# Kernel tuning notes

Measured on AMD Instinct MI355X. Metric: run time of the kernel, lower is better.

## Reference

```python
import jax, jax.numpy as jnp
import numpy as np

E = 256
CH = 16  # channel rows; features viewed as (16,16)


def _sigmoid_np(x):
    return 1.0 / (1.0 + np.exp(-x))


def _schedule(emb, comp_l, comp_r, cb, seqs):
    """Phase 1 (host/numpy, mirrors the detached torch control flow):
    runs the iterative argmax-merge tree construction and records the
    integer merge schedule (new composed node pairs per iteration) and the
    (target, ctx_left, ctx_right) prediction triples. Matches Banyan.compose."""
    emb = np.asarray(emb, np.float32)
    sl = _sigmoid_np(np.asarray(comp_l, np.float32))
    sr = _sigmoid_np(np.asarray(comp_r, np.float32))
    cbn = np.asarray(cb, np.float32)
    seqs = np.asarray(seqs, np.int64)

    uniq = np.unique(seqs)
    lookup = np.zeros(uniq.max() + 1, np.int64)
    lookup[uniq] = np.arange(len(uniq))
    lookup[uniq[-1]] = -1  # max unique value acts as pad sentinel (lookup[-1] = -1)
    index = lookup[seqs].copy()
    tokens = uniq[:-1]

    nodes = emb[tokens]  # detached node features used only for similarity / schedule

    def comp(f):  # f: (K,2,16,16)
        return (f[:, 0] * sl + f[:, 1] * sr + cbn).reshape(f.shape[0], -1)

    pair_src = np.zeros((0, 2), np.int64)
    pair_dst = np.zeros((0,), np.int64)
    new_pairs, targets = [], []
    B, W = index.shape

    while W != 1:
        valid = index != -1
        f = nodes[np.clip(index, 0, None)]              # (B,W,E)
        a, b = f[:, :-1], f[:, 1:]
        na = np.linalg.norm(a, axis=-1)
        nb = np.linalg.norm(b, axis=-1)
        cos = (a * b).sum(-1) / np.maximum(na * nb, 1e-8)
        cos = np.where(valid[:, 1:], cos, -np.inf)       # right slot padded -> -inf
        ms_all = np.argmax(cos, axis=1)
        active = ~np.all(index[:, 1:] == -1, axis=1)
        rows = np.nonzero(active)[0]
        ms = ms_all[rows]
        lp, rp = ms, ms + 1
        src = np.stack([index[rows, lp], index[rows, rp]], 1)  # (A,2)

        # dedup against existing composed pairs, then unique new pairs (sorted)
        if pair_src.shape[0] > 0 and src.shape[0] > 0:
            exists = (src[:, None, :] == pair_src[None]).all(-1).any(1)
            newp = src[~exists]
        else:
            newp = src
        if newp.shape[0] > 0:
            newp = np.unique(newp, axis=0)
        base = nodes.shape[0]
        if newp.shape[0] > 0:
            nodes = np.concatenate([nodes, comp(nodes[newp].reshape(-1, 2, CH, CH))], 0)
            pair_src = np.concatenate([pair_src, newp], 0)
            pair_dst = np.concatenate([pair_dst, base + np.arange(newp.shape[0])], 0)
        new_pairs.append(newp.astype(np.int64))

        # neighbourhood targets (get_neighbours): l_t block then r_t block
        lefts, rights = src[:, 0], src[:, 1]
        ls = index[rows, lp - 1].copy()
        ls[lp - 1 == -1] = -1
        rs = index[rows, np.minimum(rp + 1, W - 1)].copy()
        rs[rp + 1 == W] = -2
        targets.append(np.stack([lefts, ls, rights], 1))
        targets.append(np.stack([rights, lefts, rs], 1))

        # point both merged slots at the (possibly shared) composed node id
        if src.shape[0] > 0:
            eq = (src[:, None, :] == pair_src[None]).all(-1)
            nid = pair_dst[eq.argmax(1)]
            index[rows, lp] = nid
            index[rows, rp] = nid

        # reduce frontier: active rows drop the left merge slot, inactive drop last col
        keep = np.ones_like(index, dtype=bool)
        keep[rows, ms] = False
        keep[~active, -1] = False
        index = index[keep].reshape(B, W - 1)
        W -= 1

    targets = np.concatenate(targets, 0).astype(np.int64)
    return tokens, new_pairs, targets


def _replay(emb, comp_l, comp_r, cb, sos, eos, tokens, new_pairs, targets):
    """Phase 2 (jax, differentiable): rebuild node features following the
    recorded schedule, then compute the context->target cross entropy."""
    sl = jax.nn.sigmoid(comp_l)
    sr = jax.nn.sigmoid(comp_r)
    feats = emb[tokens]                                    # (n_tok, E)
    for p in new_pairs:
        if p.shape[0] == 0:
            continue
        f = feats[p].reshape(-1, 2, CH, CH)                # (K,2,16,16)
        feats = jnp.concatenate([feats, (f[:, 0] * sl + f[:, 1] * sr + cb).reshape(-1, E)], 0)
    feats = jnp.concatenate([feats, eos[None, :], sos[None, :]], 0)
    N = feats.shape[0]
    t = np.where(targets < 0, targets + N, targets)        # wrap -1 -> sos, -2 -> eos
    l = feats[t[:, 1]].reshape(-1, CH, CH)
    r = feats[t[:, 2]].reshape(-1, CH, CH)
    outs = (l * sl + r * sr + cb).reshape(-1, E)           # (T,E)
    logits = outs @ feats.T                                # (T,N)
    logp = jax.nn.log_softmax(logits, axis=-1)
    return -jnp.mean(logp[jnp.arange(t.shape[0]), t[:, 0]])


def setup_inputs() -> dict:
    key = jax.random.key(0)
    k1, k2, k3, k4, k5, k6, k7 = jax.random.split(key, 7)
    V, B, L = 30000, 64, 64
    tok = jax.random.randint(k1, (B, L), 0, V - 1, dtype=jnp.int32)
    lengths = jax.random.randint(k2, (B,), L // 2, L + 1, dtype=jnp.int32)
    lengths = lengths.at[0].set(L // 2)  # guarantee pad token (V-1) is present
    x = jnp.where(jnp.arange(L)[None, :] < lengths[:, None], tok, V - 1)
    return {
        "x": x,
        "emb": jax.random.normal(k3, (V, E), jnp.float32),
        "comp_l": jax.random.uniform(k4, (CH,), jnp.float32, 0.6, 0.9),
        "comp_r": jax.random.uniform(k5, (CH,), jnp.float32, 0.6, 0.9),
        "cb": jnp.zeros((CH,), jnp.float32),
        "sos": 0.02 * jax.random.normal(k6, (E,), jnp.float32),
        "eos": 0.02 * jax.random.normal(k7, (E,), jnp.float32),
    }


def reference(x, emb, comp_l, comp_r, cb, sos, eos):
    tokens, new_pairs, targets = _schedule(emb, comp_l, comp_r, cb, x)
    return _replay(emb, comp_l, comp_r, cb, sos, eos, tokens, new_pairs, targets)
```

## Files before the change

### kernel.cpp

```cpp
#include <hip/hip_runtime.h>
#include <math.h>


#define NMAX 8192
#define PRES 30720
#define HBITS 13
#define HSIZE 8192
#define HMASK 8191
#define LOG2E 1.44269504f
#define LN2 0.69314718f

typedef float f32x4 __attribute__((ext_vector_type(4)));
typedef short short8 __attribute__((ext_vector_type(8)));

__device__ __forceinline__ unsigned hash0(int key) {
    return (((unsigned)key) * 2654435761u) >> (32 - HBITS);
}

__device__ __forceinline__ unsigned short f2bf(float f) {
    unsigned u = __float_as_uint(f);
    unsigned r = ((u >> 16) & 1u) + 0x7FFFu;
    return (unsigned short)((u + r) >> 16);
}

__device__ __forceinline__ float rdl_f(float v, int lane) {
    return __int_as_float(__builtin_amdgcn_readlane(__float_as_int(v), lane));
}

#define SUM_STEP(CTRL, X) \
    X += __int_as_float(__builtin_amdgcn_update_dpp(0, __float_as_int(X), CTRL, 0xF, 0xF, true));
#define SUM3_REDUCE(A, B, C) {                                                  \
    SUM_STEP(0x121, A) SUM_STEP(0x121, B) SUM_STEP(0x121, C)                    \
    SUM_STEP(0x122, A) SUM_STEP(0x122, B) SUM_STEP(0x122, C)                    \
    SUM_STEP(0x124, A) SUM_STEP(0x124, B) SUM_STEP(0x124, C)                    \
    SUM_STEP(0x128, A) SUM_STEP(0x128, B) SUM_STEP(0x128, C)                    \
    A = rdl_f(A, 0) + rdl_f(A, 16) + rdl_f(A, 32) + rdl_f(A, 48);               \
    B = rdl_f(B, 0) + rdl_f(B, 16) + rdl_f(B, 32) + rdl_f(B, 48);               \
    C = rdl_f(C, 0) + rdl_f(C, 16) + rdl_f(C, 32) + rdl_f(C, 48);               \
}
#define ARGMAX_STEP(CTRL, V, I) {                                               \
    float _ov = __int_as_float(__builtin_amdgcn_update_dpp(0, __float_as_int(V), CTRL, 0xF, 0xF, true)); \
    int _oi = __builtin_amdgcn_update_dpp(0, I, CTRL, 0xF, 0xF, true);          \
    if (_ov > V || (_ov == V && _oi < I)) { V = _ov; I = _oi; }                 \
}
#define ARGMAX_REDUCE(V, I) {                                                   \
    ARGMAX_STEP(0x121, V, I) ARGMAX_STEP(0x122, V, I)                           \
    ARGMAX_STEP(0x124, V, I) ARGMAX_STEP(0x128, V, I)                           \
    float _v0 = rdl_f(V, 0), _v1 = rdl_f(V, 16), _v2 = rdl_f(V, 32), _v3 = rdl_f(V, 48); \
    int _i0 = __builtin_amdgcn_readlane(I, 0), _i1 = __builtin_amdgcn_readlane(I, 16);   \
    int _i2 = __builtin_amdgcn_readlane(I, 32), _i3 = __builtin_amdgcn_readlane(I, 48);  \
    V = _v0; I = _i0;                                                           \
    if (_v1 > V || (_v1 == V && _i1 < I)) { V = _v1; I = _i1; }                 \
    if (_v2 > V || (_v2 == V && _i2 < I)) { V = _v2; I = _i2; }                 \
    if (_v3 > V || (_v3 == V && _i3 < I)) { V = _v3; I = _i3; }                 \
}

__global__ __launch_bounds__(1024) void prep_kernel(
    const int* __restrict__ x, int* __restrict__ tokens,
    int* __restrict__ meta, int* __restrict__ index_g) {
    __shared__ int pres[PRES];
    __shared__ int part[1024];
    int tid = threadIdx.x;
    for (int i = tid; i < PRES; i += 1024) pres[i] = 0;
    __syncthreads();
    for (int i = tid; i < 4096; i += 1024) pres[x[i]] = 1;
    __syncthreads();
    int base = tid * 30;
    int loc[30];
    int s = 0;
#pragma unroll
    for (int i = 0; i < 30; ++i) { loc[i] = s; s += pres[base + i]; }
    part[tid] = s;
    __syncthreads();
    for (int off = 1; off < 1024; off <<= 1) {
        int v = (tid >= off) ? part[tid - off] : 0;
        __syncthreads();
        part[tid] += v;
        __syncthreads();
    }
    int excl = (tid == 0) ? 0 : part[tid - 1];
    int total = part[1023];
#pragma unroll
    for (int i = 0; i < 30; ++i) {
        if (pres[base + i]) tokens[excl + loc[i]] = base + i;
    }
    if (tid == 0) { meta[0] = total; meta[1] = total - 1; }
    for (int i = tid; i < 4096; i += 1024) {
        int t = x[i];
        int th = t / 30;
        int b2 = th * 30, off = t - b2;
        int r = (th ? part[th - 1] : 0);
        for (int j = 0; j < off; ++j) r += pres[b2 + j];
        index_g[i] = (r == total - 1) ? -1 : r;
    }
}

__global__ void copy_feats_kernel(const float* __restrict__ emb, const int* __restrict__ tokens,
                                  const int* __restrict__ meta, float* __restrict__ feats,
                                  float* __restrict__ norms) {
    int n = blockIdx.x;
    if (n >= meta[1]) return;
    int t = tokens[n];
    int k = threadIdx.x;
    const float4* src = (const float4*)(emb + (size_t)t * 256);
    float4* dst = (float4*)(feats + (size_t)n * 256);
    float4 v = src[k];
    dst[k] = v;
    float ss = v.x * v.x + v.y * v.y + v.z * v.z + v.w * v.w;
#pragma unroll
    for (int off = 32; off >= 1; off >>= 1) ss += __shfl_down(ss, off);
    if (k == 0) norms[n] = sqrtf(ss);
}

__global__ void init_cos_kernel(const float* __restrict__ feats, const float* __restrict__ norms,
                                const int* __restrict__ index_g, float* __restrict__ cos_g) {
    int bid = blockIdx.x;
    int b = bid / 63, j = bid % 63;
    int l = index_g[b * 64 + j], r = index_g[b * 64 + j + 1];
    float c = -INFINITY;
    if (r != -1) {
        int k = threadIdx.x;
        const float4* fa = (const float4*)(feats + (size_t)l * 256);
        const float4* fb = (const float4*)(feats + (size_t)r * 256);
        float4 a = fa[k], bb = fb[k];
        float d = a.x * bb.x + a.y * bb.y + a.z * bb.z + a.w * bb.w;
#pragma unroll
        for (int off = 32; off >= 1; off >>= 1) d += __shfl_down(d, off);
        c = d / fmaxf(norms[l] * norms[r], 1e-8f);
    }
    if (threadIdx.x == 0) cos_g[b * 64 + j] = c;
}


__global__ __launch_bounds__(64) void treebuild_kernel(
    const float* __restrict__ feats, const float* __restrict__ norms_g,
    const int* __restrict__ index_g, const float* __restrict__ cos_g,
    float* __restrict__ rowfeats, int4* __restrict__ rec,
    const float* __restrict__ comp_l, const float* __restrict__ comp_r,
    const float* __restrict__ cb) {
    __shared__ float lf[127][256];
    __shared__ int4 s_rec[63];
    int b = blockIdx.x;
    int lane = threadIdx.x;
    int c0 = 4 * (lane & 3);
    float4 sl4 = make_float4(1.f / (1.f + __expf(-comp_l[c0])),
                             1.f / (1.f + __expf(-comp_l[c0 + 1])),
                             1.f / (1.f + __expf(-comp_l[c0 + 2])),
                             1.f / (1.f + __expf(-comp_l[c0 + 3])));
    float4 sr4 = make_float4(1.f / (1.f + __expf(-comp_r[c0])),
                             1.f / (1.f + __expf(-comp_r[c0 + 1])),
                             1.f / (1.f + __expf(-comp_r[c0 + 2])),
                             1.f / (1.f + __expf(-comp_r[c0 + 3])));
    float4 cb4 = make_float4(cb[c0], cb[c0 + 1], cb[c0 + 2], cb[c0 + 3]);

    int gid = index_g[b * 64 + lane];
    int isreal = (gid >= 0) ? 1 : 0;
    for (int j = 0; j < 64; ++j) {
        int g = index_g[b * 64 + j];
        int gc = g < 0 ? 0 : g;
        ((float4*)&lf[j][0])[lane] = ((const float4*)(feats + (size_t)gc * 256))[lane];
    }
    float n0 = (gid >= 0) ? norms_g[gid] : 0.f;
    float n1 = 0.f;
    float cosr = (lane < 63) ? cos_g[b * 64 + lane] : -INFINITY;
    int locid = lane;
    unsigned long long alive = ~0ull;
    int nreal = 64 - __popcll(__ballot(gid < 0));

    float Mv = cosr; int Mi = lane;
    ARGMAX_REDUCE(Mv, Mi);

    for (int it = 0; it < 63; ++it) {
        int act = (nreal >= 2) ? 1 : 0;
        int p = Mi;
        unsigned long long after = (alive >> 1) >> p;
        int q = (p + 1 + __builtin_ctzll(after | 0x8000000000000000ull)) & 63;
        unsigned long long bel = alive & ((1ull << p) - 1ull);
        int pp = bel ? (63 - __builtin_clzll(bel)) : -1;
        unsigned long long aft2 = (q < 63) ? (alive >> (q + 1)) : 0ull;
        int ssp = aft2 ? (q + 1 + __builtin_ctzll(aft2)) : -1;
        int l_loc = __builtin_amdgcn_readlane(locid, p);
        int r_loc = __builtin_amdgcn_readlane(locid, q);
        int lsl = __builtin_amdgcn_readlane(locid, pp < 0 ? 0 : pp);
        int rsl = __builtin_amdgcn_readlane(locid, ssp < 0 ? 0 : ssp);
        int ls_loc = (pp >= 0) ? lsl : -1;
        int rs_loc = (ssp >= 0) ? rsl : -2;
        int Creal = (ssp >= 0) ? __builtin_amdgcn_readlane(isreal, ssp) : 0;
        if (lane == 0)
            s_rec[it] = make_int4(act ? l_loc : -9, r_loc, ls_loc, rs_loc);
        if (act) {
            float4 a = ((const float4*)&lf[l_loc][0])[lane];
            float4 bb = ((const float4*)&lf[r_loc][0])[lane];
            float4 av = (pp >= 0) ? ((const float4*)&lf[ls_loc < 0 ? 0 : ls_loc][0])[lane]
                                  : make_float4(0.f, 0.f, 0.f, 0.f);
            float4 cv = Creal ? ((const float4*)&lf[rs_loc < 0 ? 0 : rs_loc][0])[lane]
                              : make_float4(0.f, 0.f, 0.f, 0.f);
            float mv = (lane == p || lane == q || lane == pp) ? -INFINITY : cosr;
            float Mv2 = mv; int Mi2 = lane;
            ARGMAX_REDUCE(Mv2, Mi2);
            int nl = 64 + it;
            float4 v;
            v.x = a.x * sl4.x + bb.x * sr4.x + cb4.x;
            v.y = a.y * sl4.y + bb.y * sr4.y + cb4.y;
            v.z = a.z * sl4.z + bb.z * sr4.z + cb4.z;
            v.w = a.w * sl4.w + bb.w * sr4.w + cb4.w;
            ((float4*)&lf[nl][0])[lane] = v;
            float sv = v.x * v.x + v.y * v.y + v.z * v.z + v.w * v.w;
            float da = av.x * v.x + av.y * v.y + av.z * v.z + av.w * v.w;
            float dc = cv.x * v.x + cv.y * v.y + cv.z * v.z + cv.w * v.w;
            SUM3_REDUCE(sv, da, dc);
            float nn = sqrtf(sv);
            if (lane == it) n1 = nn;
            float nA = 1.f, nC = 1.f;
            if (pp >= 0) nA = (ls_loc < 64) ? rdl_f(n0, ls_loc) : rdl_f(n1, ls_loc - 64);
            if (Creal)   nC = (rs_loc < 64) ? rdl_f(n0, rs_loc) : rdl_f(n1, rs_loc - 64);
            float cosA = da / fmaxf(nA * nn, 1e-8f);
            float cosC = Creal ? (dc / fmaxf(nn * nC, 1e-8f)) : -INFINITY;
            if (lane == p) { cosr = cosC; locid = nl; }
            if (lane == pp) cosr = cosA;
            if (lane == q) cosr = -INFINITY;
            if (pp >= 0 && (cosA > Mv2 || (cosA == Mv2 && pp < Mi2))) { Mv2 = cosA; Mi2 = pp; }
            if (cosC > Mv2 || (cosC == Mv2 && p < Mi2)) { Mv2 = cosC; Mi2 = p; }
            Mv = Mv2; Mi = Mi2;
            alive &= ~(1ull << q);
            nreal -= 1;
        }
    }
    for (int it = 0; it < 63; ++it) {
        ((float4*)(rowfeats + ((size_t)b * 63 + it) * 256))[lane] =
            ((const float4*)&lf[64 + it][0])[lane];
    }
    if (lane < 63) rec[b * 63 + lane] = s_rec[lane];
}


__global__ __launch_bounds__(64) void idassign_kernel(
    const int4* __restrict__ rec, const int* __restrict__ index_g,
    int* __restrict__ targets, int* __restrict__ meta, int* __restrict__ newsrc) {
    __shared__ int s_map[64][128];
    __shared__ int s_hk[HSIZE], s_hv[HSIZE];
    int b = threadIdx.x;
    for (int i = b; i < HSIZE; i += 64) s_hk[i] = -1;
    for (int i = b; i < 4096; i += 64) s_map[i >> 6][i & 63] = index_g[i];
    int N0 = meta[1];
    int Ncur = N0, Tcur = 0;
    __syncthreads();
    int4 R = rec[b * 63];
    for (int it = 0; it < 63; ++it) {
        int4 Rn = R;
        if (it + 1 < 63) Rn = rec[b * 63 + it + 1];
        int act = (R.x != -9) ? 1 : 0;
        int l_g = 0, r_g = 0, key = 0, nid = 0;
        int ls_g = -1, rs_g = -2;
        unsigned h = 0;
        int won = 0, need = 0;
        if (act) {
            l_g = s_map[b][R.x];
            r_g = s_map[b][R.y];
            ls_g = (R.z >= 0) ? s_map[b][R.z] : R.z;
            rs_g = (R.w >= 0) ? s_map[b][R.w] : R.w;
            key = (l_g << HBITS) | r_g;
            h = hash0(key);
            need = 1;
        }
        while (__any(need)) {
            if (need) {
                int prev = atomicCAS(&s_hk[h], -1, key);
                if (prev == -1) { won = 1; need = 0; }
                else if (prev == key) { need = 0; }
                else { h = (h + 1) & HMASK; }
            }
        }
        unsigned long long actmask = __ballot(act != 0);
        unsigned long long winmask = __ballot(won != 0);
        unsigned long long below = (1ull << b) - 1ull;
        int ar = __popcll(actmask & below);
        int nact = __popcll(actmask);
        int newc = __popcll(winmask);
        if (won) {
            nid = Ncur + __popcll(winmask & below);
            s_hv[h] = nid;
        }
        __syncthreads();
        if (act && !won) nid = s_hv[h];
        if (won) newsrc[nid - N0] = (b << 6) | it;
        if (act) {
            int o1 = Tcur + ar;
            targets[o1 * 3 + 0] = l_g;
            targets[o1 * 3 + 1] = ls_g;
            targets[o1 * 3 + 2] = r_g;
            int o2 = Tcur + nact + ar;
            targets[o2 * 3 + 0] = r_g;
            targets[o2 * 3 + 1] = l_g;
            targets[o2 * 3 + 2] = rs_g;
            s_map[b][64 + it] = nid;
        }
        Ncur += newc;
        Tcur += 2 * nact;
        R = Rn;
    }
    if (b == 0) { meta[2] = Ncur; meta[3] = Tcur; meta[4] = Ncur - N0; }
}


__global__ __launch_bounds__(64) void materialize_kernel(
    const float* __restrict__ rowfeats, const int* __restrict__ newsrc,
    const int* __restrict__ meta, float* __restrict__ feats,
    const float* __restrict__ eos, const float* __restrict__ sos) {
    int g = blockIdx.x;
    int lane = threadIdx.x;
    if (g == 4032) {
        int n = meta[2];
        ((float4*)(feats + (size_t)n * 256))[lane] = ((const float4*)eos)[lane];
        ((float4*)(feats + (size_t)(n + 1) * 256))[lane] = ((const float4*)sos)[lane];
        return;
    }
    if (g >= meta[4]) return;
    int pk = newsrc[g];
    int b = pk >> 6, it = pk & 63;
    int N0 = meta[1];
    ((float4*)(feats + (size_t)(N0 + g) * 256))[lane] =
        ((const float4*)(rowfeats + ((size_t)b * 63 + it) * 256))[lane];
}

__global__ __launch_bounds__(256) void convert_feats_kernel(
    const float* __restrict__ feats, short8* __restrict__ fhT) {
    int g = blockIdx.x * 256 + threadIdx.x;
    int tile = g >> 9, rem = g & 511;
    int ks = rem >> 6, lane64 = rem & 63;
    int kq = lane64 >> 4, col = lane64 & 15;
    int row = tile * 16 + col;
    int e0 = (ks * 4 + kq) * 8;
    const float4* src = (const float4*)(feats + (size_t)row * 256 + e0);
    float4 v0 = src[0], v1 = src[1];
    short8 o;
    o[0] = (short)f2bf(v0.x); o[1] = (short)f2bf(v0.y);
    o[2] = (short)f2bf(v0.z); o[3] = (short)f2bf(v0.w);
    o[4] = (short)f2bf(v1.x); o[5] = (short)f2bf(v1.y);
    o[6] = (short)f2bf(v1.z); o[7] = (short)f2bf(v1.w);
    fhT[g] = o;
}

__global__ __launch_bounds__(256) void prep_outs_kernel(
    const float* __restrict__ feats, const int* __restrict__ targets,
    const int* __restrict__ meta, const float* __restrict__ comp_l,
    const float* __restrict__ comp_r, const float* __restrict__ cb,
    unsigned short* __restrict__ oh, float* __restrict__ tdot) {
    int T = meta[3];
    int Ntot = meta[2] + 2;
    int t = blockIdx.x * 4 + (threadIdx.x >> 6);
    if (t >= T) return;
    int lane = threadIdx.x & 63;
    int c0 = 4 * (lane & 3);
    float4 sl4 = make_float4(1.f / (1.f + __expf(-comp_l[c0])),
                             1.f / (1.f + __expf(-comp_l[c0 + 1])),
                             1.f / (1.f + __expf(-comp_l[c0 + 2])),
                             1.f / (1.f + __expf(-comp_l[c0 + 3])));
    float4 sr4 = make_float4(1.f / (1.f + __expf(-comp_r[c0])),
                             1.f / (1.f + __expf(-comp_r[c0 + 1])),
                             1.f / (1.f + __expf(-comp_r[c0 + 2])),
                             1.f / (1.f + __expf(-comp_r[c0 + 3])));
    float4 cb4 = make_float4(cb[c0], cb[c0 + 1], cb[c0 + 2], cb[c0 + 3]);
    int t0 = targets[t * 3 + 0];
    int i1 = targets[t * 3 + 1], i2 = targets[t * 3 + 2];
    if (i1 < 0) i1 += Ntot;
    if (i2 < 0) i2 += Ntot;
    float4 a = ((const float4*)(feats + (size_t)i1 * 256))[lane];
    float4 b = ((const float4*)(feats + (size_t)i2 * 256))[lane];
    float4 ft = ((const float4*)(feats + (size_t)t0 * 256))[lane];
    float4 v;
    v.x = a.x * sl4.x + b.x * sr4.x + cb4.x;
    v.y = a.y * sl4.y + b.y * sr4.y + cb4.y;
    v.z = a.z * sl4.z + b.z * sr4.z + cb4.z;
    v.w = a.w * sl4.w + b.w * sr4.w + cb4.w;
    float d = v.x * ft.x + v.y * ft.y + v.z * ft.z + v.w * ft.w;
#pragma unroll
    for (int off = 32; off >= 1; off >>= 1) d += __shfl_down(d, off);
    if (lane == 0) tdot[t] = d;
    ushort4 h;
    h.x = f2bf(v.x); h.y = f2bf(v.y); h.z = f2bf(v.z); h.w = f2bf(v.w);
    ((ushort4*)(oh + (size_t)t * 256))[lane] = h;
}

__global__ __launch_bounds__(512) void loss_mfma_kernel(
    const short8* __restrict__ fhT, const unsigned short* __restrict__ oh,
    const int* __restrict__ meta, float2* __restrict__ partial) {
    __shared__ float s_m[64][2], s_s[64][2];
    int T = meta[3];
    int Ntot = meta[2] + 2;
    int row0 = blockIdx.x * 64;
    if (row0 >= T) return;
    int slab = blockIdx.y;
    int P = (Ntot + 127) >> 7;
    int cstart = slab * (P << 5);
    int cend = min(Ntot, cstart + (P << 5));
    int tid = threadIdx.x, lane = tid & 63, w = tid >> 6;
    int mq = w >> 1, nq = w & 1;
    int mrow = row0 + mq * 16 + (lane & 15);
    int kq = lane >> 4;
    const short8* pah = (const short8*)(oh + (size_t)mrow * 256);
    short8 Ah[8];
#pragma unroll
    for (int ks = 0; ks < 8; ++ks) Ah[ks] = pah[ks * 4 + kq];
    float m0 = -1e30f, m1 = -1e30f, m2 = -1e30f, m3 = -1e30f;
    float s0 = 0.f, s1 = 0.f, s2 = 0.f, s3 = 0.f;
    for (int nb = cstart; nb < cend; nb += 32) {
        const short8* pb = fhT + ((size_t)(nb >> 4) + nq) * 512;
        f32x4 a0 = {0.f, 0.f, 0.f, 0.f}, a1 = a0;
#pragma unroll
        for (int ks = 0; ks < 4; ++ks) {
            a0 = __builtin_amdgcn_mfma_f32_16x16x32_bf16(Ah[ks], pb[ks * 64 + lane], a0, 0, 0, 0);
            a1 = __builtin_amdgcn_mfma_f32_16x16x32_bf16(Ah[ks + 4], pb[(ks + 4) * 64 + lane], a1, 0, 0, 0);
        }
        int col = nb + nq * 16 + (lane & 15);
        bool cv = col < cend;
        float v0 = cv ? (a0[0] + a1[0]) * LOG2E : -INFINITY;
        float v1 = cv ? (a0[1] + a1[1]) * LOG2E : -INFINITY;
        float v2 = cv ? (a0[2] + a1[2]) * LOG2E : -INFINITY;
        float v3 = cv ? (a0[3] + a1[3]) * LOG2E : -INFINITY;
        if (v0 > m0) { s0 = s0 * exp2f(m0 - v0) + 1.f; m0 = v0; } else s0 += exp2f(v0 - m0);
        if (v1 > m1) { s1 = s1 * exp2f(m1 - v1) + 1.f; m1 = v1; } else s1 += exp2f(v1 - m1);
        if (v2 > m2) { s2 = s2 * exp2f(m2 - v2) + 1.f; m2 = v2; } else s2 += exp2f(v2 - m2);
        if (v3 > m3) { s3 = s3 * exp2f(m3 - v3) + 1.f; m3 = v3; } else s3 += exp2f(v3 - m3);
    }
#pragma unroll
    for (int off = 1; off < 16; off <<= 1) {
        float mo, so, mn;
        mo = __shfl_xor(m0, off); so = __shfl_xor(s0, off);
        mn = fmaxf(m0, mo); s0 = s0 * exp2f(m0 - mn) + so * exp2f(mo - mn); m0 = mn;
        mo = __shfl_xor(m1, off); so = __shfl_xor(s1, off);
        mn = fmaxf(m1, mo); s1 = s1 * exp2f(m1 - mn) + so * exp2f(mo - mn); m1 = mn;
        mo = __shfl_xor(m2, off); so = __shfl_xor(s2, off);
        mn = fmaxf(m2, mo); s2 = s2 * exp2f(m2 - mn) + so * exp2f(mo - mn); m2 = mn;
        mo = __shfl_xor(m3, off); so = __shfl_xor(s3, off);
        mn = fmaxf(m3, mo); s3 = s3 * exp2f(m3 - mn) + so * exp2f(mo - mn); m3 = mn;
    }
    if ((lane & 15) == 0) {
        int rbase = mq * 16 + kq * 4;
        s_m[rbase + 0][nq] = m0; s_s[rbase + 0][nq] = s0;
        s_m[rbase + 1][nq] = m1; s_s[rbase + 1][nq] = s1;
        s_m[rbase + 2][nq] = m2; s_s[rbase + 2][nq] = s2;
        s_m[rbase + 3][nq] = m3; s_s[rbase + 3][nq] = s3;
    }
    __syncthreads();
    if (tid < 64) {
        float ma = s_m[tid][0], mb = s_m[tid][1];
        float mn = fmaxf(ma, mb);
        float ss = s_s[tid][0] * exp2f(ma - mn) + s_s[tid][1] * exp2f(mb - mn);
        partial[(size_t)slab * NMAX + row0 + tid] = make_float2(mn, ss);
    }
}

__global__ __launch_bounds__(1024) void combine_kernel(
    const float2* __restrict__ partial, const float* __restrict__ tdot,
    const int* __restrict__ meta, float* __restrict__ out) {
    __shared__ float red[16];
    int T = meta[3];
    float loss = 0.f;
    for (int r = threadIdx.x; r < T; r += 1024) {
        float2 p0 = partial[r];
        float2 p1 = partial[NMAX + r];
        float2 p2 = partial[2 * NMAX + r];
        float2 p3 = partial[3 * NMAX + r];
        float mn = fmaxf(fmaxf(p0.x, p1.x), fmaxf(p2.x, p3.x));
        float ss = p0.y * exp2f(p0.x - mn) + p1.y * exp2f(p1.x - mn) +
                   p2.y * exp2f(p2.x - mn) + p3.y * exp2f(p3.x - mn);
        loss += (mn + __log2f(ss)) * LN2 - tdot[r];
    }
#pragma unroll
    for (int off = 32; off >= 1; off >>= 1) loss += __shfl_down(loss, off);
    if ((threadIdx.x & 63) == 0) red[threadIdx.x >> 6] = loss;
    __syncthreads();
    if (threadIdx.x < 16) {
        loss = red[threadIdx.x];
#pragma unroll
        for (int off = 8; off >= 1; off >>= 1) loss += __shfl_down(loss, off);
        if (threadIdx.x == 0) out[0] = loss / (float)T;
    }
}

extern "C" void kernel_launch(void* const* d_in, const int* in_sizes, int n_in,
                              void* d_out, int out_size, void* d_ws, size_t ws_size,
                              hipStream_t stream) {
    const int* x = (const int*)d_in[0];
    const float* emb = (const float*)d_in[1];
    const float* comp_l = (const float*)d_in[2];
    const float* comp_r = (const float*)d_in[3];
    const float* cb = (const float*)d_in[4];
    const float* sos = (const float*)d_in[5];
    const float* eos = (const float*)d_in[6];
    float* out = (float*)d_out;

    float* feats = (float*)d_ws;
    float* norms = feats + (size_t)NMAX * 256;
    int* index_g = (int*)(norms + NMAX);
    float* cos_g = (float*)(index_g + 4096);
    int* tokens = (int*)(cos_g + 4096);
    int* targets = tokens + 4096;
    int* meta = targets + NMAX * 3;
    float* tdot = (float*)(meta + 64);
    float2* partial = (float2*)(tdot + NMAX);
    int4* rec = (int4*)(partial + 4 * NMAX);
    int* newsrc = (int*)(rec + 64 * 63);
    float* rowfeats = (float*)(newsrc + 4096);
    short8* fhT = (short8*)(rowfeats + (size_t)64 * 63 * 256);
    unsigned short* oh = (unsigned short*)(fhT + (size_t)NMAX * 32);

    prep_kernel<<<1, 1024, 0, stream>>>(x, tokens, meta, index_g);
    copy_feats_kernel<<<4096, 64, 0, stream>>>(emb, tokens, meta, feats, norms);
    init_cos_kernel<<<64 * 63, 64, 0, stream>>>(feats, norms, index_g, cos_g);
    treebuild_kernel<<<64, 64, 0, stream>>>(feats, norms, index_g, cos_g,
                                            rowfeats, rec, comp_l, comp_r, cb);
    idassign_kernel<<<1, 64, 0, stream>>>(rec, index_g, targets, meta, newsrc);
    materialize_kernel<<<4033, 64, 0, stream>>>(rowfeats, newsrc, meta, feats, eos, sos);
    convert_feats_kernel<<<1024, 256, 0, stream>>>(feats, fhT);
    prep_outs_kernel<<<2016, 256, 0, stream>>>(feats, targets, meta, comp_l, comp_r,
                                               cb, oh, tdot);
    loss_mfma_kernel<<<dim3(126, 4), 512, 0, stream>>>(fhT, oh, meta, partial);
    combine_kernel<<<1, 1024, 0, stream>>>(partial, tdot, meta, out);
}
```

Before: 218.5 us.

## Replace index prefix loop with table lookup, use fast reciprocal, retile loss MFMA kernel

New measurement: 264.6 us. +21.1%, slower.

```diff
diff --git a/kernel.cpp b/kernel.cpp
--- a/kernel.cpp
+++ b/kernel.cpp
@@ -85,12 +85,12 @@
         if (pres[base + i]) tokens[excl + loc[i]] = base + i;
     }
     if (tid == 0) { meta[0] = total; meta[1] = total - 1; }
+    __syncthreads();
+#pragma unroll
+    for (int i = 0; i < 30; ++i) pres[base + i] = excl + loc[i];
+    __syncthreads();
     for (int i = tid; i < 4096; i += 1024) {
-        int t = x[i];
-        int th = t / 30;
-        int b2 = th * 30, off = t - b2;
-        int r = (th ? part[th - 1] : 0);
-        for (int j = 0; j < off; ++j) r += pres[b2 + j];
+        int r = pres[x[i]];
         index_g[i] = (r == total - 1) ? -1 : r;
     }
 }
@@ -214,8 +214,8 @@
             float nA = 1.f, nC = 1.f;
             if (pp >= 0) nA = (ls_loc < 64) ? rdl_f(n0, ls_loc) : rdl_f(n1, ls_loc - 64);
             if (Creal)   nC = (rs_loc < 64) ? rdl_f(n0, rs_loc) : rdl_f(n1, rs_loc - 64);
-            float cosA = da / fmaxf(nA * nn, 1e-8f);
-            float cosC = Creal ? (dc / fmaxf(nn * nC, 1e-8f)) : -INFINITY;
+            float cosA = da * __builtin_amdgcn_rcpf(fmaxf(nA * nn, 1e-8f));
+            float cosC = Creal ? (dc * __builtin_amdgcn_rcpf(fmaxf(nn * nC, 1e-8f))) : -INFINITY;
             if (lane == p) { cosr = cosC; locid = nl; }
             if (lane == pp) cosr = cosA;
             if (lane == q) cosr = -INFINITY;
@@ -385,35 +385,34 @@
 __global__ __launch_bounds__(512) void loss_mfma_kernel(
     const short8* __restrict__ fhT, const unsigned short* __restrict__ oh,
     const int* __restrict__ meta, float2* __restrict__ partial) {
-    __shared__ float s_m[64][2], s_s[64][2];
     int T = meta[3];
     int Ntot = meta[2] + 2;
-    int row0 = blockIdx.x * 64;
+    int row0 = blockIdx.x * 128;
     if (row0 >= T) return;
     int slab = blockIdx.y;
-    int P = (Ntot + 127) >> 7;
-    int cstart = slab * (P << 5);
-    int cend = min(Ntot, cstart + (P << 5));
+    int P16 = (Ntot + 63) >> 6;
+    int cstart = slab * (P16 << 4);
+    int cend = min(Ntot, cstart + (P16 << 4));
     int tid = threadIdx.x, lane = tid & 63, w = tid >> 6;
-    int mq = w >> 1, nq = w & 1;
-    int mrow = row0 + mq * 16 + (lane & 15);
+    int mrowb = row0 + w * 16;
+    int mrow = mrowb + (lane & 15);
+    int mrowc = min(mrow, T - 1);
     int kq = lane >> 4;
-    const short8* pah = (const short8*)(oh + (size_t)mrow * 256);
+    const short8* pah = (const short8*)(oh + (size_t)mrowc * 256);
     short8 Ah[8];
 #pragma unroll
     for (int ks = 0; ks < 8; ++ks) Ah[ks] = pah[ks * 4 + kq];
     float m0 = -1e30f, m1 = -1e30f, m2 = -1e30f, m3 = -1e30f;
     float s0 = 0.f, s1 = 0.f, s2 = 0.f, s3 = 0.f;
-    for (int nb = cstart; nb < cend; nb += 32) {
-        const short8* pb = fhT + ((size_t)(nb >> 4) + nq) * 512;
+    for (int nb = cstart; nb < cend; nb += 16) {
+        const short8* pb = fhT + ((size_t)(nb >> 4)) * 512;
         f32x4 a0 = {0.f, 0.f, 0.f, 0.f}, a1 = a0;
 #pragma unroll
         for (int ks = 0; ks < 4; ++ks) {
             a0 = __builtin_amdgcn_mfma_f32_16x16x32_bf16(Ah[ks], pb[ks * 64 + lane], a0, 0, 0, 0);
             a1 = __builtin_amdgcn_mfma_f32_16x16x32_bf16(Ah[ks + 4], pb[(ks + 4) * 64 + lane], a1, 0, 0, 0);
         }
-        int col = nb + nq * 16 + (lane & 15);
-        bool cv = col < cend;
+        bool cv = (nb + (lane & 15)) < cend;
         float v0 = cv ? (a0[0] + a1[0]) * LOG2E : -INFINITY;
         float v1 = cv ? (a0[1] + a1[1]) * LOG2E : -INFINITY;
         float v2 = cv ? (a0[2] + a1[2]) * LOG2E : -INFINITY;
@@ -436,18 +435,11 @@
         mn = fmaxf(m3, mo); s3 = s3 * exp2f(m3 - mn) + so * exp2f(mo - mn); m3 = mn;
     }
     if ((lane & 15) == 0) {
-        int rbase = mq * 16 + kq * 4;
-        s_m[rbase + 0][nq] = m0; s_s[rbase + 0][nq] = s0;
-        s_m[rbase + 1][nq] = m1; s_s[rbase + 1][nq] = s1;
-        s_m[rbase + 2][nq] = m2; s_s[rbase + 2][nq] = s2;
-        s_m[rbase + 3][nq] = m3; s_s[rbase + 3][nq] = s3;
-    }
-    __syncthreads();
-    if (tid < 64) {
-        float ma = s_m[tid][0], mb = s_m[tid][1];
-        float mn = fmaxf(ma, mb);
-        float ss = s_s[tid][0] * exp2f(ma - mn) + s_s[tid][1] * exp2f(mb - mn);
-        partial[(size_t)slab * NMAX + row0 + tid] = make_float2(mn, ss);
+        int rb = mrowb + kq * 4;
+        if (rb + 0 < T) partial[(size_t)slab * NMAX + rb + 0] = make_float2(m0, s0);
+        if (rb + 1 < T) partial[(size_t)slab * NMAX + rb + 1] = make_float2(m1, s1);
+        if (rb + 2 < T) partial[(size_t)slab * NMAX + rb + 2] = make_float2(m2, s2);
+        if (rb + 3 < T) partial[(size_t)slab * NMAX + rb + 3] = make_float2(m3, s3);
     }
 }
 
@@ -516,6 +508,6 @@
     convert_feats_kernel<<<1024, 256, 0, stream>>>(feats, fhT);
     prep_outs_kernel<<<2016, 256, 0, stream>>>(feats, targets, meta, comp_l, comp_r,
                                                cb, oh, tdot);
-    loss_mfma_kernel<<<dim3(126, 4), 512, 0, stream>>>(fhT, oh, meta, partial);
+    loss_mfma_kernel<<<dim3(63, 4), 512, 0, stream>>>(fhT, oh, meta, partial);
     combine_kernel<<<1, 1024, 0, stream>>>(partial, tdot, meta, out);
 }
```
